# Performance work log

Measured on AMD Instinct MI355X. Metric: run time of the kernel, lower is better.

## Reference

```python
import jax, jax.numpy as jnp
import numpy as np

NUM_LAYERS = 2
VOCAB = 32000
IN_FEAT = 256          # embedding dim is IN_FEAT-1, +1 for cue scalar
HIDDEN = 256
ATN = 64               # hardcoded atn_feature_size in GraphConvolution
CLASSES = 2
B, N = 8, 2048


def setup_inputs() -> dict:
    key = jax.random.key(0)
    ks = jax.random.split(key, 12)
    x = jax.random.randint(ks[0], (B, N), 0, VOCAB, dtype=jnp.int32)
    cue = jax.random.randint(ks[1], (B, N), 0, 2, dtype=jnp.int32)
    adj = (jax.random.uniform(ks[2], (B, N, N)) < 0.01).astype(jnp.float32)
    s = 1.0 / np.sqrt(HIDDEN)
    emb_table = jax.random.normal(ks[3], (VOCAB, IN_FEAT - 1), jnp.float32) * 0.02
    Wh = jax.random.uniform(ks[4], (IN_FEAT, HIDDEN), jnp.float32, -s, s)
    bh = jax.random.uniform(ks[5], (HIDDEN,), jnp.float32, -s, s)
    Wq = jax.random.uniform(ks[6], (HIDDEN, ATN), jnp.float32, -s, s)
    Wk = jax.random.uniform(ks[7], (HIDDEN, ATN), jnp.float32, -s, s)
    Wv = jax.random.uniform(ks[8], (HIDDEN, HIDDEN), jnp.float32, -s, s)
    gcb = jax.random.uniform(ks[9], (HIDDEN,), jnp.float32, -s, s)
    Wc = jax.random.uniform(ks[10], (HIDDEN, CLASSES), jnp.float32, -s, s)
    bc = jax.random.uniform(ks[11], (CLASSES,), jnp.float32, -s, s)
    return {"x": x, "cue": cue, "adj": adj, "emb_table": emb_table,
            "Wh": Wh, "bh": bh, "Wq": Wq, "Wk": Wk, "Wv": Wv,
            "gcb": gcb, "Wc": Wc, "bc": bc}


def graph_attention_layer(h, adj, Wq, Wk, Wv, gcb):
    # h: [B,N,H]; adj: [B,N,N] binary. Per node i: softmax over neighbors j of
    # (Wk h_j) . (Wq h_i), weighted sum of Wv h_j. Zero-degree nodes get 0 (pre-bias).
    q = jnp.einsum('bnh,ha->bna', h, Wq)        # [B,N,A]
    k = jnp.einsum('bnh,ha->bna', h, Wk)        # [B,N,A]
    v = jnp.einsum('bnh,hg->bng', h, Wv)        # [B,N,H]
    logits = jnp.einsum('bia,bja->bij', q, k)   # [B,N,N]
    mask = adj > 0
    attn = jax.nn.softmax(jnp.where(mask, logits, -1e9), axis=-1)
    out = jnp.einsum('bij,bjh->bih', attn, v)   # [B,N,H]
    has_nbr = jnp.any(mask, axis=-1, keepdims=True)  # [B,N,1]
    return jnp.where(has_nbr, out, 0.0) + gcb


def reference(x, cue, adj, emb_table, Wh, bh, Wq, Wk, Wv, gcb, Wc, bc):
    emb = emb_table[x]                                   # [B,N,IN_FEAT-1]
    feats = jnp.concatenate([emb, cue.astype(jnp.float32)[..., None]], axis=-1)
    h = jax.nn.relu(jnp.einsum('bnf,fh->bnh', feats, Wh) + bh)
    for _ in range(NUM_LAYERS):
        h = jax.nn.sigmoid(graph_attention_layer(h, adj, Wq, Wk, Wv, gcb))
    logits = jnp.einsum('bnh,hc->bnc', h, Wc) + bc
    return jax.nn.softmax(logits, axis=-1)
```

## Files before the change

kernel.cpp:

```cpp
#include <hip/hip_runtime.h>
#include <hip/hip_bf16.h>


#define NB 8
#define NN 2048
#define ROWS (NB * NN)
#define MAXD 64

typedef float f4 __attribute__((ext_vector_type(4)));
typedef short bf8 __attribute__((ext_vector_type(8)));
typedef unsigned short u16;
typedef u16 us4 __attribute__((ext_vector_type(4)));
typedef u16 us8 __attribute__((ext_vector_type(8)));

__device__ __forceinline__ float sigmoidf_(float x) { return 1.f / (1.f + __expf(-x)); }
__device__ __forceinline__ u16 f2bf(float f) {
    unsigned u = __float_as_uint(f);
    u += 0x7fffu + ((u >> 16) & 1u);
    return (u16)(u >> 16);
}
__device__ __forceinline__ float bf2f(u16 h) {
    return __uint_as_float(((unsigned)h) << 16);
}

#define PACK_BLKS 96
#define EMB_BLKS 512

__global__ __launch_bounds__(256) void k_fused_front(
        const int* __restrict__ x, const int* __restrict__ cue,
        const float* __restrict__ adj, const float* __restrict__ emb,
        const float* __restrict__ Wh, const float* __restrict__ bh,
        const float* __restrict__ Wq, const float* __restrict__ Wk,
        const float* __restrict__ Wv,
        u16* __restrict__ hB, u16* __restrict__ Wpt,
        int* __restrict__ deg, int* __restrict__ nbr) {
    __shared__ float As[32 * 64];
    __shared__ float Ws[32 * 128];
    int bid = blockIdx.x;
    int t = threadIdx.x;

    if (bid < PACK_BLKS) {
        int idxp = bid * 256 + t;
#pragma unroll
        for (int r = 0; r < 4; ++r) {
            int i = idxp + r * PACK_BLKS * 256;
            int c = i >> 8, f = i & 255;
            float v;
            if (c < 64)       v = Wq[f * 64 + c];
            else if (c < 128) v = Wk[f * 64 + (c - 64)];
            else              v = Wv[f * 256 + (c - 128)];
            Wpt[i] = f2bf(v);
        }
        return;
    }

    if (bid < PACK_BLKS + EMB_BLKS) {
        int rb2 = bid - PACK_BLKS;
        int v2 = ((rb2 & 7) << 6) + (rb2 >> 3);
        int rt = v2 >> 1, ct = v2 & 1;
        int row0 = rt * 64, col0 = ct * 128;
        int sm = t & 63, skg = t >> 6;
        int swc = (t & 31) * 4, swk = t >> 5;
        int tx = t & 15, ty = t >> 4;
        int xr = x[row0 + sm];
        float cv = (float)cue[row0 + sm];
        const float* er = emb + (size_t)xr * 255;

        float acc[4][8];
#pragma unroll
        for (int i = 0; i < 4; ++i)
#pragma unroll
            for (int j = 0; j < 8; ++j) acc[i][j] = 0.f;

        for (int kc = 0; kc < 256; kc += 32) {
            int kb = skg * 8;
#pragma unroll
            for (int u = 0; u < 8; ++u) {
                int f = kc + kb + u;
                As[(kb + u) * 64 + sm] = (f < 255) ? er[f] : cv;
            }
#pragma unroll
            for (int r = 0; r < 4; ++r) {
                int kk = swk + r * 8;
                f4 w = *(const f4*)(Wh + (size_t)(kc + kk) * 256 + col0 + swc);
                *(f4*)&Ws[kk * 128 + swc] = w;
            }
            __syncthreads();
#pragma unroll
            for (int k = 0; k < 32; ++k) {
                f4 av = *(f4*)&As[k * 64 + ty * 4];
                f4 w0 = *(f4*)&Ws[k * 128 + tx * 8];
                f4 w1 = *(f4*)&Ws[k * 128 + tx * 8 + 4];
                float a[4] = {av.x, av.y, av.z, av.w};
                float w[8] = {w0.x, w0.y, w0.z, w0.w, w1.x, w1.y, w1.z, w1.w};
#pragma unroll
                for (int i = 0; i < 4; ++i)
#pragma unroll
                    for (int j = 0; j < 8; ++j) acc[i][j] += a[i] * w[j];
            }
            __syncthreads();
        }
        f4 b0 = *(const f4*)(bh + col0 + tx * 8);
        f4 b1 = *(const f4*)(bh + col0 + tx * 8 + 4);
        float bb[8] = {b0.x, b0.y, b0.z, b0.w, b1.x, b1.y, b1.z, b1.w};
#pragma unroll
        for (int i = 0; i < 4; ++i) {
            int row = row0 + ty * 4 + i;
            us8 o;
#pragma unroll
            for (int j = 0; j < 8; ++j) o[j] = f2bf(fmaxf(acc[i][j] + bb[j], 0.f));
            *(us8*)(hB + (size_t)row * 256 + col0 + tx * 8) = o;
        }
        return;
    }

    int rb = bid - (PACK_BLKS + EMB_BLKS);
    int row = ((rb & 7) << 11) + (rb >> 3);
    const f4* ar4 = (const f4*)(adj + (size_t)row * NN);
    int* cnt = (int*)As;
    if (t == 0) *cnt = 0;
    __syncthreads();
    int* nr = nbr + (size_t)row * MAXD;
#pragma unroll
    for (int it = 0; it < 2; ++it) {
        int idx = it * 256 + t;
        f4 vv = __builtin_nontemporal_load(ar4 + idx);
        if (vv.x > 0.f) { int p = atomicAdd(cnt, 1); if (p < MAXD) nr[p] = idx * 4 + 0; }
        if (vv.y > 0.f) { int p = atomicAdd(cnt, 1); if (p < MAXD) nr[p] = idx * 4 + 1; }
        if (vv.z > 0.f) { int p = atomicAdd(cnt, 1); if (p < MAXD) nr[p] = idx * 4 + 2; }
        if (vv.w > 0.f) { int p = atomicAdd(cnt, 1); if (p < MAXD) nr[p] = idx * 4 + 3; }
    }
    __syncthreads();
    int c = *cnt; if (c > MAXD) c = MAXD;
    if (t == 0) deg[row] = c;
    if (t < MAXD && t >= c) nr[t] = 0;
}

__global__ __launch_bounds__(256) void k_qkv_mfma(const u16* __restrict__ hB,
                                                  const u16* __restrict__ Wpt,
                                                  float* __restrict__ q,
                                                  u16* __restrict__ kv) {
    __shared__ u16 As[64 * 40];
    __shared__ u16 Bs[128 * 40];
    int t = threadIdx.x;
    int flat = blockIdx.x + blockIdx.y * 3;
    int v = ((flat & 7) * 96) + (flat >> 3);
    int col0 = (v % 3) * 128, row0 = (v / 3) * 64;
    int wave = t >> 6, lane = t & 63;
    int l16 = lane & 15, quad = lane >> 4;

    f4 acc[4][2];
#pragma unroll
    for (int i = 0; i < 4; ++i) { acc[i][0] = (f4){0,0,0,0}; acc[i][1] = (f4){0,0,0,0}; }

    int ar = t >> 2, ao = (t & 3) * 8;
    int bc = t >> 1, bo = (t & 1) * 16;
    const u16* aP = hB  + (size_t)(row0 + ar) * 256 + ao;
    const u16* bP = Wpt + (size_t)(col0 + bc) * 256 + bo;

    us8 av  = *(const us8*)(aP);
    us8 bv0 = *(const us8*)(bP);
    us8 bv1 = *(const us8*)(bP + 8);

#pragma unroll
    for (int kc = 0; kc < 256; kc += 32) {
        __syncthreads();
        *(us8*)&As[ar * 40 + ao] = av;
        *(us8*)&Bs[bc * 40 + bo] = bv0;
        *(us8*)&Bs[bc * 40 + bo + 8] = bv1;
        __syncthreads();
        if (kc + 32 < 256) {
            av  = *(const us8*)(aP + kc + 32);
            bv0 = *(const us8*)(bP + kc + 32);
            bv1 = *(const us8*)(bP + kc + 40);
        }
        bf8 afr[4], bfr[2];
#pragma unroll
        for (int mt = 0; mt < 4; ++mt)
            afr[mt] = *(bf8*)&As[(mt * 16 + l16) * 40 + quad * 8];
#pragma unroll
        for (int nt = 0; nt < 2; ++nt)
            bfr[nt] = *(bf8*)&Bs[((wave * 2 + nt) * 16 + l16) * 40 + quad * 8];
#pragma unroll
        for (int mt = 0; mt < 4; ++mt)
#pragma unroll
            for (int nt = 0; nt < 2; ++nt)
                acc[mt][nt] = __builtin_amdgcn_mfma_f32_16x16x32_bf16(
                    afr[mt], bfr[nt], acc[mt][nt], 0, 0, 0);
    }
#pragma unroll
    for (int mt = 0; mt < 4; ++mt)
#pragma unroll
        for (int nt = 0; nt < 2; ++nt) {
            int c = col0 + (wave * 2 + nt) * 16 + l16;
#pragma unroll
            for (int reg = 0; reg < 4; ++reg) {
                int r = row0 + mt * 16 + quad * 4 + reg;
                float val = acc[mt][nt][reg];
                if (c < 64) q[(size_t)r * 64 + c] = val * 1.44269504f;
                else        kv[(size_t)r * 320 + (c - 64)] = f2bf(val);
            }
        }
}

template <bool WRITE_OUT>
__global__ __launch_bounds__(256) void k_attn(const float* __restrict__ q,
                                              const u16* __restrict__ kv,
                                              const int* __restrict__ deg,
                                              const int* __restrict__ nbr,
                                              const float* __restrict__ gcb,
                                              const float* __restrict__ Wc,
                                              const float* __restrict__ bc,
                                              u16* __restrict__ hB,
                                              float* __restrict__ out) {
    int wave = threadIdx.x >> 6;
    int lane = threadIdx.x & 63;
    int bid = blockIdx.x;
    int vb = ((bid & 7) << 9) + (bid >> 3);
    int row = vb * 4 + wave;
    int d = deg[row];
    int l16 = lane & 15;
    int g = lane >> 4;
    f4 g4 = *(const f4*)(gcb + lane * 4);
    float h0, h1, h2, h3;
    if (d == 0) {
        h0 = sigmoidf_(g4.x); h1 = sigmoidf_(g4.y);
        h2 = sigmoidf_(g4.z); h3 = sigmoidf_(g4.w);
    } else {
        f4 q4 = *(const f4*)(q + (size_t)row * 64 + l16 * 4);
        const int* jl = nbr + (size_t)row * MAXD;
        const u16* kvb = kv + (size_t)(row & ~(NN - 1)) * 320;
        int gx1 = g ^ 1, gx2 = g ^ 2, gx3 = g ^ 3;
        float s = 0.f;
        f4 a = {0, 0, 0, 0};
        int j0 = jl[g], j1 = jl[gx1], j2 = jl[gx2], j3 = jl[gx3];
        us4 kq = *(const us4*)(kvb + (size_t)j0 * 320 + l16 * 4);
        for (int e = 0; e < d; e += 4) {
            int en = (e + 4 < d) ? (e + 4) : 0;
            int j0n = jl[en + g],   j1n = jl[en + gx1];
            int j2n = jl[en + gx2], j3n = jl[en + gx3];
            us4 kqn = *(const us4*)(kvb + (size_t)j0n * 320 + l16 * 4);
            us4 u0 = *(const us4*)(kvb + (size_t)j0 * 320 + 64 + lane * 4);
            us4 u1 = *(const us4*)(kvb + (size_t)j1 * 320 + 64 + lane * 4);
            us4 u2 = *(const us4*)(kvb + (size_t)j2 * 320 + 64 + lane * 4);
            us4 u3 = *(const us4*)(kvb + (size_t)j3 * 320 + 64 + lane * 4);
            float p = q4.x * bf2f(kq.x) + q4.y * bf2f(kq.y)
                    + q4.z * bf2f(kq.z) + q4.w * bf2f(kq.w);
            p += __shfl_xor(p, 1); p += __shfl_xor(p, 2);
            p += __shfl_xor(p, 4); p += __shfl_xor(p, 8);
            if (e + g >= d) p = -1e30f;
            float w = __builtin_amdgcn_exp2f(p);
            float wa = __shfl_xor(w, 16);
            float wb = __shfl_xor(w, 32);
            float wc = __shfl_xor(wa, 32);
            s += (w + wa) + (wb + wc);
            a.x += w * bf2f(u0.x) + wa * bf2f(u1.x) + wb * bf2f(u2.x) + wc * bf2f(u3.x);
            a.y += w * bf2f(u0.y) + wa * bf2f(u1.y) + wb * bf2f(u2.y) + wc * bf2f(u3.y);
            a.z += w * bf2f(u0.z) + wa * bf2f(u1.z) + wb * bf2f(u2.z) + wc * bf2f(u3.z);
            a.w += w * bf2f(u0.w) + wa * bf2f(u1.w) + wb * bf2f(u2.w) + wc * bf2f(u3.w);
            j0 = j0n; j1 = j1n; j2 = j2n; j3 = j3n; kq = kqn;
        }
        float inv = 1.f / s;
        h0 = sigmoidf_(a.x * inv + g4.x);
        h1 = sigmoidf_(a.y * inv + g4.y);
        h2 = sigmoidf_(a.z * inv + g4.z);
        h3 = sigmoidf_(a.w * inv + g4.w);
    }
    if (!WRITE_OUT) {
        us4 o;
        o.x = f2bf(h0); o.y = f2bf(h1); o.z = f2bf(h2); o.w = f2bf(h3);
        *(us4*)(hB + (size_t)row * 256 + lane * 4) = o;
    } else {
        f4 wc0 = *(const f4*)(Wc + lane * 8);
        f4 wc1 = *(const f4*)(Wc + lane * 8 + 4);
        float pa = h0 * wc0.x + h1 * wc0.z + h2 * wc1.x + h3 * wc1.z;
        float pb = h0 * wc0.y + h1 * wc0.w + h2 * wc1.y + h3 * wc1.w;
#pragma unroll
        for (int off = 32; off; off >>= 1) {
            pa += __shfl_xor(pa, off);
            pb += __shfl_xor(pb, off);
        }
        if (lane == 0) {
            float l0 = pa + bc[0], l1 = pb + bc[1];
            float mx = fmaxf(l0, l1);
            float e0 = __expf(l0 - mx), e1 = __expf(l1 - mx);
            float inv = 1.f / (e0 + e1);
            out[(size_t)row * 2 + 0] = e0 * inv;
            out[(size_t)row * 2 + 1] = e1 * inv;
        }
    }
}

extern "C" void kernel_launch(void* const* d_in, const int* in_sizes, int n_in,
                              void* d_out, int out_size, void* d_ws, size_t ws_size,
                              hipStream_t stream) {
    const int*   x    = (const int*)d_in[0];
    const int*   cue  = (const int*)d_in[1];
    const float* adj  = (const float*)d_in[2];
    const float* emb  = (const float*)d_in[3];
    const float* Wh   = (const float*)d_in[4];
    const float* bh   = (const float*)d_in[5];
    const float* Wq   = (const float*)d_in[6];
    const float* Wk   = (const float*)d_in[7];
    const float* Wv   = (const float*)d_in[8];
    const float* gcb  = (const float*)d_in[9];
    const float* Wc   = (const float*)d_in[10];
    const float* bc   = (const float*)d_in[11];
    float* out = (float*)d_out;

    char* w = (char*)d_ws;
    u16*   hB  = (u16*)w;                 w += (size_t)ROWS * 256 * 2;
    float* q   = (float*)w;               w += (size_t)ROWS * 64 * 4;
    u16*   kv  = (u16*)w;                 w += (size_t)ROWS * 320 * 2;
    u16*   Wpt = (u16*)w;                 w += (size_t)384 * 256 * 2;
    int*   deg = (int*)w;                 w += (size_t)ROWS * 4;
    int*   nbr = (int*)w;

    k_fused_front<<<PACK_BLKS + EMB_BLKS + ROWS, 256, 0, stream>>>(
        x, cue, adj, emb, Wh, bh, Wq, Wk, Wv, hB, Wpt, deg, nbr);
    k_qkv_mfma<<<dim3(3, ROWS / 64), 256, 0, stream>>>(hB, Wpt, q, kv);
    k_attn<false><<<ROWS / 4, 256, 0, stream>>>(q, kv, deg, nbr, gcb, Wc, bc, hB, out);
    k_qkv_mfma<<<dim3(3, ROWS / 64), 256, 0, stream>>>(hB, Wpt, q, kv);
    k_attn<true><<<ROWS / 4, 256, 0, stream>>>(q, kv, deg, nbr, gcb, Wc, bc, hB, out);
}
```

Before: 322.8 us.

## Use bf16 MFMA for embedding projection GEMM with register-prefetched inputs

Replaces the fp32 FMA tiled GEMM in the embedding-projection blocks of the fused front kernel with bf16 MFMA 16x16x32 instructions. The A tile is converted to bf16 into padded shared memory, while the Wh fragments are read straight from global memory and converted per lane, so the Ws shared tile goes away. The next k-chunk of embedding values is prefetched into registers to overlap the gathers. The change trades fp32 precision for bf16 inputs on this GEMM, and it adds strided uncoalesced Wh loads and scattered 2-byte output stores.

```diff
diff --git a/kernel.cpp b/kernel.cpp
--- a/kernel.cpp
+++ b/kernel.cpp
@@ -35,7 +35,6 @@
         u16* __restrict__ hB, u16* __restrict__ Wpt,
         int* __restrict__ deg, int* __restrict__ nbr) {
     __shared__ float As[32 * 64];
-    __shared__ float Ws[32 * 128];
     int bid = blockIdx.x;
     int t = threadIdx.x;
 
@@ -59,57 +58,71 @@
         int v2 = ((rb2 & 7) << 6) + (rb2 >> 3);
         int rt = v2 >> 1, ct = v2 & 1;
         int row0 = rt * 64, col0 = ct * 128;
-        int sm = t & 63, skg = t >> 6;
-        int swc = (t & 31) * 4, swk = t >> 5;
-        int tx = t & 15, ty = t >> 4;
+        int sm = t & 63, skg = t >> 6, kb = skg * 8;
+        int wave = t >> 6, lane = t & 63;
+        int l16 = lane & 15, quad = lane >> 4;
         int xr = x[row0 + sm];
         float cv = (float)cue[row0 + sm];
         const float* er = emb + (size_t)xr * 255;
-
-        float acc[4][8];
-#pragma unroll
-        for (int i = 0; i < 4; ++i)
-#pragma unroll
-            for (int j = 0; j < 8; ++j) acc[i][j] = 0.f;
-
+        u16* Asb = (u16*)As;
+
+        f4 acc[4][2];
+#pragma unroll
+        for (int i = 0; i < 4; ++i) { acc[i][0] = (f4){0,0,0,0}; acc[i][1] = (f4){0,0,0,0}; }
+
+        float fv[8];
+#pragma unroll
+        for (int u = 0; u < 8; ++u) {
+            int f = kb + u;
+            fv[u] = (f < 255) ? er[f] : cv;
+        }
+
+#pragma unroll
         for (int kc = 0; kc < 256; kc += 32) {
-            int kb = skg * 8;
-#pragma unroll
-            for (int u = 0; u < 8; ++u) {
-                int f = kc + kb + u;
-                As[(kb + u) * 64 + sm] = (f < 255) ? er[f] : cv;
+            us8 a8;
+#pragma unroll
+            for (int u = 0; u < 8; ++u) a8[u] = f2bf(fv[u]);
+            __syncthreads();
+            *(us8*)&Asb[sm * 40 + kb] = a8;
+            __syncthreads();
+            if (kc + 32 < 256) {
+#pragma unroll
+                for (int u = 0; u < 8; ++u) {
+                    int f = kc + 32 + kb + u;
+                    fv[u] = (f < 255) ? er[f] : cv;
+                }
             }
-#pragma unroll
-            for (int r = 0; r < 4; ++r) {
-                int kk = swk + r * 8;
-                f4 w = *(const f4*)(Wh + (size_t)(kc + kk) * 256 + col0 + swc);
-                *(f4*)&Ws[kk * 128 + swc] = w;
+            bf8 bfr[2];
+#pragma unroll
+            for (int nt = 0; nt < 2; ++nt) {
+                int n = col0 + (wave * 2 + nt) * 16 + l16;
+                const float* wp = Wh + (size_t)(kc + quad * 8) * 256 + n;
+#pragma unroll
+                for (int j = 0; j < 8; ++j)
+                    bfr[nt][j] = (short)f2bf(wp[(size_t)j * 256]);
             }
-            __syncthreads();
-#pragma unroll
-            for (int k = 0; k < 32; ++k) {
-                f4 av = *(f4*)&As[k * 64 + ty * 4];
-                f4 w0 = *(f4*)&Ws[k * 128 + tx * 8];
-                f4 w1 = *(f4*)&Ws[k * 128 + tx * 8 + 4];
-                float a[4] = {av.x, av.y, av.z, av.w};
-                float w[8] = {w0.x, w0.y, w0.z, w0.w, w1.x, w1.y, w1.z, w1.w};
-#pragma unroll
-                for (int i = 0; i < 4; ++i)
-#pragma unroll
-                    for (int j = 0; j < 8; ++j) acc[i][j] += a[i] * w[j];
-            }
-            __syncthreads();
-        }
-        f4 b0 = *(const f4*)(bh + col0 + tx * 8);
-        f4 b1 = *(const f4*)(bh + col0 + tx * 8 + 4);
-        float bb[8] = {b0.x, b0.y, b0.z, b0.w, b1.x, b1.y, b1.z, b1.w};
-#pragma unroll
-        for (int i = 0; i < 4; ++i) {
-            int row = row0 + ty * 4 + i;
-            us8 o;
-#pragma unroll
-            for (int j = 0; j < 8; ++j) o[j] = f2bf(fmaxf(acc[i][j] + bb[j], 0.f));
-            *(us8*)(hB + (size_t)row * 256 + col0 + tx * 8) = o;
+            bf8 afr[4];
+#pragma unroll
+            for (int mt = 0; mt < 4; ++mt)
+                afr[mt] = *(bf8*)&Asb[(mt * 16 + l16) * 40 + quad * 8];
+#pragma unroll
+            for (int mt = 0; mt < 4; ++mt)
+#pragma unroll
+                for (int nt = 0; nt < 2; ++nt)
+                    acc[mt][nt] = __builtin_amdgcn_mfma_f32_16x16x32_bf16(
+                        afr[mt], bfr[nt], acc[mt][nt], 0, 0, 0);
+        }
+#pragma unroll
+        for (int nt = 0; nt < 2; ++nt) {
+            int c = col0 + (wave * 2 + nt) * 16 + l16;
+            float bb = bh[c];
+#pragma unroll
+            for (int mt = 0; mt < 4; ++mt)
+#pragma unroll
+                for (int reg = 0; reg < 4; ++reg) {
+                    int r = row0 + mt * 16 + quad * 4 + reg;
+                    hB[(size_t)r * 256 + c] = f2bf(fmaxf(acc[mt][nt][reg] + bb, 0.f));
+                }
         }
         return;
     }
```

After: 326.4 us. About the same (+1.1%).
